# Optimization experiments

Measured on AMD Instinct MI355X. Metric: run time of the kernel, lower is better.

## Reference

```python
import jax, jax.numpy as jnp
import numpy as np
import math

TAU = math.log(2.0)   # C=2
LAM = 0.25
BATCH_SIZE = 12


def _lambertw(y, iters=20):
    """Principal-branch Lambert W for y >= -1/e via Halley iteration (on-device,
    replacing the scipy CPU roundtrip)."""
    # initial guess: series expansion near the branch point, log1p elsewhere
    w = jnp.where(
        y < 1.0,
        -1.0 + jnp.sqrt(jnp.maximum(2.0 * (jnp.e * y + 1.0), 0.0)),
        jnp.log1p(y),
    )

    def body(w, _):
        ew = jnp.exp(w)
        f = w * ew - y
        denom = ew * (w + 1.0) - (w + 2.0) * f / (2.0 * (w + 1.0) + 1e-12)
        w = jnp.where(jnp.abs(f) > 0.0, w - f / denom, w)
        return w, None

    w, _ = jax.lax.scan(body, w, None, length=iters)
    return w


def setup_inputs() -> dict:
    key = jax.random.key(0)
    n = 2097152  # rows per label group
    logits = jax.random.normal(key, (3 * n, 3), dtype=jnp.float32)
    return {"discriminator_out": logits, "n0": n, "n1": n, "n2": n}


def reference(discriminator_out, n0, n1, n2):
    # labels: n0 zeros, n1 ones, n2 twos (static sizes)
    labels = jnp.concatenate([
        jnp.zeros((n0,), jnp.int32),
        jnp.ones((n1,), jnp.int32),
        jnp.full((n2,), 2, jnp.int32),
    ])
    # per-row cross entropy (single log_softmax shared by both CE uses in the torch code)
    logp = jax.nn.log_softmax(discriminator_out, axis=-1)
    l_i = -jnp.take_along_axis(logp, labels[:, None], axis=1)[:, 0]  # [N]

    # sigma uses detached losses
    l_det = jax.lax.stop_gradient(l_i)
    y = 0.5 * jnp.maximum(-2.0 / jnp.e, (l_det - TAU) / LAM)  # y >= -1/e
    w = _lambertw(y)
    sigma = jnp.exp(-w)  # log(sigma) = -w

    loss = ((l_i - TAU) * sigma + LAM * jnp.square(w)).sum() / BATCH_SIZE
    return loss
```

## Files before the change

### kernel.cpp

```cpp
#include <hip/hip_runtime.h>
#include <math.h>

#define TBL_N     1024
#define KIDX      44.36141955583649f
#define LOG2E     1.44269504088896340736f
#define INV_BATCH (1.0f / 12.0f)

struct TblData { float v[TBL_N + 1]; };

constexpr double k_ln2 = 0.69314718055994530942;
constexpr double k_e   = 2.71828182845904523536;

constexpr double cexp(double x) {
    double t = x * 1.44269504088896340736;
    int n = (int)(t + (t >= 0 ? 0.5 : -0.5));
    double r = x - (double)n * k_ln2;
    double s = 1.0, term = 1.0;
    for (int i = 1; i <= 13; ++i) { term *= r / i; s += term; }
    double p = 1.0;
    if (n >= 0) for (int i = 0; i <  n; ++i) p *= 2.0;
    else        for (int i = 0; i < -n; ++i) p *= 0.5;
    return s * p;
}
constexpr double csqrt_(double x) {
    double r = x > 1.0 ? x : 1.0;
    for (int i = 0; i < 24; ++i) r = 0.5 * (r + x / r);
    return r;
}
constexpr double clog_(double x) {
    int n = 0; double m = x;
    while (m >= 2.0) { m *= 0.5; ++n; }
    while (m <  1.0) { m *= 2.0; --n; }
    double z = (m - 1.0) / (m + 1.0), z2 = z * z, s = 0.0, t = z;
    for (int i = 0; i < 17; ++i) { s += t / (2 * i + 1); t *= z2; }
    return 2.0 * s + (double)n * k_ln2;
}
constexpr TblData make_table() {
    TblData T{};
    for (int i = 0; i <= TBL_N; ++i) {
        double l   = (double)i * (16.0 / TBL_N);
        double tau = k_ln2;
        double l0  = tau - 1.0 / (2.0 * k_e);
        double F;
        if (l < l0) {
            F = k_e * (l - tau) + 0.25;
        } else {
            double y = 2.0 * (l - tau);
            double ylim = -1.0 / k_e;
            if (y < ylim) y = ylim;
            double w = (y < 3.0) ? (csqrt_(2.0 * (k_e * y + 1.0)) - 1.0)
                                 : clog_(y);
            for (int it = 0; it < 4; ++it) {
                double ew  = cexp(w);
                double f   = w * ew - y;
                double wp1 = w + 1.0;
                double den = ew * wp1 - (w + 2.0) * f / (2.0 * wp1 + 1e-300);
                if (f != 0.0) w -= f / den;
            }
            F = 0.25 * ((1.0 + w) * (1.0 + w) - 1.0);
        }
        T.v[i] = (float)F;
    }
    return T;
}
__device__ __constant__ TblData c_tbl = make_table();

__shared__ float s_tbl[TBL_N + 1];

__device__ __forceinline__ float row_fast(float a, float b, float c, int label) {
    float a2 = a * LOG2E, b2 = b * LOG2E, c2 = c * LOG2E;
    float s  = exp2f(a2) + exp2f(b2) + exp2f(c2);
    float xl2 = (label == 0) ? a2 : ((label == 1) ? b2 : c2);
    float u = (__log2f(s) - xl2) * KIDX;
    u = fminf(fmaxf(u, 0.0f), (float)TBL_N - 0.001f);
    int   i = (int)u;
    float f = u - (float)i;
    float t0 = s_tbl[i];
    float t1 = s_tbl[i + 1];
    return fmaf(f, t1 - t0, t0);
}

__device__ __forceinline__ float block_reduce(float acc) {
#pragma unroll
    for (int off = 32; off > 0; off >>= 1)
        acc += __shfl_down(acc, off, 64);
    __shared__ float sacc[4];
    int lane = threadIdx.x & 63;
    int wv   = threadIdx.x >> 6;
    if (lane == 0) sacc[wv] = acc;
    __syncthreads();
    float s = 0.0f;
    if (threadIdx.x == 0)
        s = sacc[0] + sacc[1] + sacc[2] + sacc[3];
    return s;
}

__global__ __launch_bounds__(256) void superloss_partial(
        const float* __restrict__ x,
        const int* __restrict__ pn0,
        const int* __restrict__ pn1,
        float* __restrict__ partial,
        int nrows) {
    for (int i = threadIdx.x; i <= TBL_N; i += 256)
        s_tbl[i] = c_tbl.v[i];
    __syncthreads();

    const int n0  = *pn0;
    const int n01 = n0 + *pn1;

    const int nq     = nrows >> 2;
    const int gid    = blockIdx.x * blockDim.x + threadIdx.x;
    const int stride = gridDim.x * blockDim.x;

    float acc = 0.0f;

    for (int q = gid; q < nq; q += stride) {
        const float4* p = (const float4*)x + 3 * (size_t)q;
        float4 f0 = p[0];
        float4 f1 = p[1];
        float4 f2 = p[2];
        int r0 = q << 2;
        int l0 = (r0     >= n0) + (r0     >= n01);
        int l1 = (r0 + 1 >= n0) + (r0 + 1 >= n01);
        int l2 = (r0 + 2 >= n0) + (r0 + 2 >= n01);
        int l3 = (r0 + 3 >= n0) + (r0 + 3 >= n01);
        acc += row_fast(f0.x, f0.y, f0.z, l0);
        acc += row_fast(f0.w, f1.x, f1.y, l1);
        acc += row_fast(f1.z, f1.w, f2.x, l2);
        acc += row_fast(f2.y, f2.z, f2.w, l3);
    }

    for (int r = (nq << 2) + gid; r < nrows; r += stride) {
        float a = x[3 * (size_t)r];
        float b = x[3 * (size_t)r + 1];
        float c = x[3 * (size_t)r + 2];
        int lab = (r >= n0) + (r >= n01);
        acc += row_fast(a, b, c, lab);
    }

    float s = block_reduce(acc);
    if (threadIdx.x == 0)
        partial[blockIdx.x] = s;
}

__global__ __launch_bounds__(256) void superloss_final(
        const float* __restrict__ partial,
        int np,
        float* __restrict__ out) {
    float acc = 0.0f;
    for (int i = threadIdx.x; i < np; i += 256)
        acc += partial[i];
    float s = block_reduce(acc);
    if (threadIdx.x == 0)
        out[0] = s * INV_BATCH;
}

extern "C" void kernel_launch(void* const* d_in, const int* in_sizes, int n_in,
                              void* d_out, int out_size, void* d_ws, size_t ws_size,
                              hipStream_t stream) {
    const float* x   = (const float*)d_in[0];
    const int*   pn0 = (const int*)d_in[1];
    const int*   pn1 = (const int*)d_in[2];

    const int nrows = in_sizes[0] / 3;

    int nblk = 2048;
    size_t need = (size_t)nblk * sizeof(float);
    if (ws_size < need) {
        nblk = (int)(ws_size / sizeof(float));
        if (nblk < 1) nblk = 1;
    }

    float* partial = (float*)d_ws;
    superloss_partial<<<nblk, 256, 0, stream>>>(x, pn0, pn1, partial, nrows);
    superloss_final<<<1, 256, 0, stream>>>(partial, nblk, (float*)d_out);
}
```

Baseline: 107.6 us.

## Specialize per-label row loops and batch three segment loads per iteration

Splits the row loop into three concurrent streams, one per label segment, each using a compile-time label so the per-row label comparisons and selects go away. Cross-entropy is reformulated as log2(1 + exp(o1-xl) + exp(o2-xl)), which drops one exp and the lower clamp. Each iteration issues loads from all three segments before computing, which puts more memory requests in flight per thread. A scalar fallback covers unaligned segment sizes; the price is higher register pressure and three separate access streams.

```diff
diff --git a/kernel.cpp b/kernel.cpp
--- a/kernel.cpp
+++ b/kernel.cpp
@@ -2,6 +2,7 @@
 #include <math.h>
 
 #define TBL_N     1024
+#define TBL_MAXU  1023.999f
 #define KIDX      44.36141955583649f
 #define LOG2E     1.44269504088896340736f
 #define INV_BATCH (1.0f / 12.0f)
@@ -67,17 +68,40 @@
 
 __shared__ float s_tbl[TBL_N + 1];
 
-__device__ __forceinline__ float row_fast(float a, float b, float c, int label) {
-    float a2 = a * LOG2E, b2 = b * LOG2E, c2 = c * LOG2E;
-    float s  = exp2f(a2) + exp2f(b2) + exp2f(c2);
-    float xl2 = (label == 0) ? a2 : ((label == 1) ? b2 : c2);
-    float u = (__log2f(s) - xl2) * KIDX;
-    u = fminf(fmaxf(u, 0.0f), (float)TBL_N - 0.001f);
+__device__ __forceinline__ float tbl_eval(float u) {
+    u = fminf(u, TBL_MAXU);
     int   i = (int)u;
     float f = u - (float)i;
     float t0 = s_tbl[i];
     float t1 = s_tbl[i + 1];
     return fmaf(f, t1 - t0, t0);
+}
+
+template<int L>
+__device__ __forceinline__ float row_fixed(float a, float b, float c) {
+    float xl = (L == 0) ? a : ((L == 1) ? b : c);
+    float o1 = (L == 0) ? b : a;
+    float o2 = (L == 2) ? b : c;
+    float e1 = exp2f((o1 - xl) * LOG2E);
+    float e2 = exp2f((o2 - xl) * LOG2E);
+    float u  = __log2f(1.0f + e1 + e2) * KIDX;
+    return tbl_eval(u);
+}
+
+__device__ __forceinline__ float row_gen(float a, float b, float c, int lab) {
+    float xl = (lab == 0) ? a : ((lab == 1) ? b : c);
+    float o1 = (lab == 0) ? b : a;
+    float o2 = (lab == 2) ? b : c;
+    float e1 = exp2f((o1 - xl) * LOG2E);
+    float e2 = exp2f((o2 - xl) * LOG2E);
+    float u  = __log2f(1.0f + e1 + e2) * KIDX;
+    return tbl_eval(u);
+}
+
+template<int L>
+__device__ __forceinline__ float quad_sum(float4 f0, float4 f1, float4 f2) {
+    return row_fixed<L>(f0.x, f0.y, f0.z) + row_fixed<L>(f0.w, f1.x, f1.y)
+         + row_fixed<L>(f1.z, f1.w, f2.x) + row_fixed<L>(f2.y, f2.z, f2.w);
 }
 
 __device__ __forceinline__ float block_reduce(float acc) {
@@ -108,34 +132,38 @@
     const int n0  = *pn0;
     const int n01 = n0 + *pn1;
 
+    const int gid    = blockIdx.x * 256 + threadIdx.x;
+    const int stride = gridDim.x * 256;
     const int nq     = nrows >> 2;
-    const int gid    = blockIdx.x * blockDim.x + threadIdx.x;
-    const int stride = gridDim.x * blockDim.x;
 
     float acc = 0.0f;
 
-    for (int q = gid; q < nq; q += stride) {
-        const float4* p = (const float4*)x + 3 * (size_t)q;
-        float4 f0 = p[0];
-        float4 f1 = p[1];
-        float4 f2 = p[2];
-        int r0 = q << 2;
-        int l0 = (r0     >= n0) + (r0     >= n01);
-        int l1 = (r0 + 1 >= n0) + (r0 + 1 >= n01);
-        int l2 = (r0 + 2 >= n0) + (r0 + 2 >= n01);
-        int l3 = (r0 + 3 >= n0) + (r0 + 3 >= n01);
-        acc += row_fast(f0.x, f0.y, f0.z, l0);
-        acc += row_fast(f0.w, f1.x, f1.y, l1);
-        acc += row_fast(f1.z, f1.w, f2.x, l2);
-        acc += row_fast(f2.y, f2.z, f2.w, l3);
-    }
-
-    for (int r = (nq << 2) + gid; r < nrows; r += stride) {
-        float a = x[3 * (size_t)r];
-        float b = x[3 * (size_t)r + 1];
-        float c = x[3 * (size_t)r + 2];
-        int lab = (r >= n0) + (r >= n01);
-        acc += row_fast(a, b, c, lab);
+    if (((n0 | n01) & 3) == 0) {
+        const int nq0 = n0 >> 2, nq1 = n01 >> 2;
+        int q0 = gid, q1 = nq0 + gid, q2 = nq1 + gid;
+        for (;;) {
+            bool h0 = q0 < nq0, h1 = q1 < nq1, h2 = q2 < nq;
+            if (!(h0 || h1 || h2)) break;
+            float4 A0, A1, A2, B0, B1, B2, C0, C1, C2;
+            if (h0) { const float4* p = (const float4*)x + 3 * (size_t)q0; A0 = p[0]; A1 = p[1]; A2 = p[2]; }
+            if (h1) { const float4* p = (const float4*)x + 3 * (size_t)q1; B0 = p[0]; B1 = p[1]; B2 = p[2]; }
+            if (h2) { const float4* p = (const float4*)x + 3 * (size_t)q2; C0 = p[0]; C1 = p[1]; C2 = p[2]; }
+            if (h0) acc += quad_sum<0>(A0, A1, A2);
+            if (h1) acc += quad_sum<1>(B0, B1, B2);
+            if (h2) acc += quad_sum<2>(C0, C1, C2);
+            q0 += stride; q1 += stride; q2 += stride;
+        }
+        for (int r = (nq << 2) + gid; r < nrows; r += stride) {
+            int lab = (r >= n0) + (r >= n01);
+            acc += row_gen(x[3 * (size_t)r], x[3 * (size_t)r + 1],
+                           x[3 * (size_t)r + 2], lab);
+        }
+    } else {
+        for (int r = gid; r < nrows; r += stride) {
+            int lab = (r >= n0) + (r >= n01);
+            acc += row_gen(x[3 * (size_t)r], x[3 * (size_t)r + 1],
+                           x[3 * (size_t)r + 2], lab);
+        }
     }
 
     float s = block_reduce(acc);
```

Result: no change. 109.1 us (+1.4%).

## Stage row tiles through LDS for coalesced loads and simplify per-row math

Applied to the files above, without the earlier changes.

Each block now loads a 1024-row tile with fully coalesced float4 reads, stages it in shared memory, then has each thread read back its own four rows. This replaces the strided 48-byte-per-thread global access. The per-row log-sum-exp now uses two exponentials relative to the label logit instead of three. The 1/12 scale is folded into the table, which removes the final multiply and the clamp at zero. The price is two barriers per tile and extra LDS traffic.

```diff
diff --git a/kernel.cpp b/kernel.cpp
--- a/kernel.cpp
+++ b/kernel.cpp
@@ -2,9 +2,12 @@
 #include <math.h>
 
 #define TBL_N     1024
+#define TBL_MAXU  1023.999f
 #define KIDX      44.36141955583649f
-#define LOG2E     1.44269504088896340736f
-#define INV_BATCH (1.0f / 12.0f)
+#define INV_BATCH (1.0 / 12.0)
+
+#define ROWS_PER_TILE 1024
+#define F4_PER_TILE   768
 
 struct TblData { float v[TBL_N + 1]; };
 
@@ -59,25 +62,30 @@
             }
             F = 0.25 * ((1.0 + w) * (1.0 + w) - 1.0);
         }
-        T.v[i] = (float)F;
+        T.v[i] = (float)(F * INV_BATCH);
     }
     return T;
 }
 __device__ __constant__ TblData c_tbl = make_table();
 
-__shared__ float s_tbl[TBL_N + 1];
-
-__device__ __forceinline__ float row_fast(float a, float b, float c, int label) {
-    float a2 = a * LOG2E, b2 = b * LOG2E, c2 = c * LOG2E;
-    float s  = exp2f(a2) + exp2f(b2) + exp2f(c2);
-    float xl2 = (label == 0) ? a2 : ((label == 1) ? b2 : c2);
-    float u = (__log2f(s) - xl2) * KIDX;
-    u = fminf(fmaxf(u, 0.0f), (float)TBL_N - 0.001f);
+__device__ __forceinline__ float tbl_eval(const float* __restrict__ tbl, float u) {
+    u = fminf(u, TBL_MAXU);
     int   i = (int)u;
     float f = u - (float)i;
-    float t0 = s_tbl[i];
-    float t1 = s_tbl[i + 1];
+    float t0 = tbl[i];
+    float t1 = tbl[i + 1];
     return fmaf(f, t1 - t0, t0);
+}
+
+__device__ __forceinline__ float row_eval(const float* __restrict__ tbl,
+                                          float a, float b, float c, int lab) {
+    float xl = (lab == 0) ? a : ((lab == 1) ? b : c);
+    float o1 = (lab == 0) ? b : a;
+    float o2 = (lab == 2) ? b : c;
+    float e1 = __expf(o1 - xl);
+    float e2 = __expf(o2 - xl);
+    float u  = __log2f(1.0f + e1 + e2) * KIDX;
+    return tbl_eval(tbl, u);
 }
 
 __device__ __forceinline__ float block_reduce(float acc) {
@@ -101,41 +109,52 @@
         const int* __restrict__ pn1,
         float* __restrict__ partial,
         int nrows) {
-    for (int i = threadIdx.x; i <= TBL_N; i += 256)
+    __shared__ float  s_tbl[TBL_N + 1];
+    __shared__ float4 s_buf[F4_PER_TILE];
+
+    const int tid = threadIdx.x;
+    for (int i = tid; i <= TBL_N; i += 256)
         s_tbl[i] = c_tbl.v[i];
-    __syncthreads();
 
     const int n0  = *pn0;
     const int n01 = n0 + *pn1;
 
-    const int nq     = nrows >> 2;
-    const int gid    = blockIdx.x * blockDim.x + threadIdx.x;
-    const int stride = gridDim.x * blockDim.x;
-
+    const int ntiles = nrows / ROWS_PER_TILE;
     float acc = 0.0f;
 
-    for (int q = gid; q < nq; q += stride) {
-        const float4* p = (const float4*)x + 3 * (size_t)q;
-        float4 f0 = p[0];
-        float4 f1 = p[1];
-        float4 f2 = p[2];
-        int r0 = q << 2;
-        int l0 = (r0     >= n0) + (r0     >= n01);
-        int l1 = (r0 + 1 >= n0) + (r0 + 1 >= n01);
-        int l2 = (r0 + 2 >= n0) + (r0 + 2 >= n01);
-        int l3 = (r0 + 3 >= n0) + (r0 + 3 >= n01);
-        acc += row_fast(f0.x, f0.y, f0.z, l0);
-        acc += row_fast(f0.w, f1.x, f1.y, l1);
-        acc += row_fast(f1.z, f1.w, f2.x, l2);
-        acc += row_fast(f2.y, f2.z, f2.w, l3);
+    for (int tile = blockIdx.x; tile < ntiles; tile += gridDim.x) {
+        const float4* src = (const float4*)x + (size_t)tile * F4_PER_TILE;
+        float4 v0 = src[tid];
+        float4 v1 = src[tid + 256];
+        float4 v2 = src[tid + 512];
+        __syncthreads();
+        s_buf[tid]       = v0;
+        s_buf[tid + 256] = v1;
+        s_buf[tid + 512] = v2;
+        __syncthreads();
+
+        float4 q0 = s_buf[3 * tid];
+        float4 q1 = s_buf[3 * tid + 1];
+        float4 q2 = s_buf[3 * tid + 2];
+
+        int r = tile * ROWS_PER_TILE + 4 * tid;
+        int l0 = (r     >= n0) + (r     >= n01);
+        int l1 = (r + 1 >= n0) + (r + 1 >= n01);
+        int l2 = (r + 2 >= n0) + (r + 2 >= n01);
+        int l3 = (r + 3 >= n0) + (r + 3 >= n01);
+
+        acc += row_eval(s_tbl, q0.x, q0.y, q0.z, l0);
+        acc += row_eval(s_tbl, q0.w, q1.x, q1.y, l1);
+        acc += row_eval(s_tbl, q1.z, q1.w, q2.x, l2);
+        acc += row_eval(s_tbl, q2.y, q2.z, q2.w, l3);
     }
 
-    for (int r = (nq << 2) + gid; r < nrows; r += stride) {
-        float a = x[3 * (size_t)r];
-        float b = x[3 * (size_t)r + 1];
-        float c = x[3 * (size_t)r + 2];
+    const int gid    = blockIdx.x * 256 + tid;
+    const int stride = gridDim.x * 256;
+    for (int r = ntiles * ROWS_PER_TILE + gid; r < nrows; r += stride) {
         int lab = (r >= n0) + (r >= n01);
-        acc += row_fast(a, b, c, lab);
+        acc += row_eval(s_tbl, x[3 * (size_t)r], x[3 * (size_t)r + 1],
+                        x[3 * (size_t)r + 2], lab);
     }
 
     float s = block_reduce(acc);
@@ -152,7 +171,7 @@
         acc += partial[i];
     float s = block_reduce(acc);
     if (threadIdx.x == 0)
-        out[0] = s * INV_BATCH;
+        out[0] = s;
 }
 
 extern "C" void kernel_launch(void* const* d_in, const int* in_sizes, int n_in,
```

Result: no change. 108.8 us (+1.1%).
